# Performance work log

Hardware: AMD Instinct MI355X
Metric: run time of the kernel (lower is better)

## Reference

```python
import jax, jax.numpy as jnp
import numpy as np

D = 256          # B == num_experts == hidden_dim == input_dim (required by the module's broadcasting)
NUM_HEADS = 4
LN_EPS = 1e-5


def _layer_norm(x, g, b):
    mu = jnp.mean(x, axis=-1, keepdims=True)
    var = jnp.mean(jnp.square(x - mu), axis=-1, keepdims=True)
    return (x - mu) * jax.lax.rsqrt(var + LN_EPS) * g + b


def setup_inputs() -> dict:
    key = jax.random.key(0)
    ks = jax.random.split(key, 12)
    B = E = H = IN = D
    s = 0.02
    return {
        "x": jax.random.normal(ks[0], (B, IN), jnp.float32),
        "task_embedding": jax.random.normal(ks[1], (B, H), jnp.float32),
        # stacked per-expert params: Linear(IN,H) -> LayerNorm(H) -> ReLU -> Linear(H,H)
        "W1": jax.random.normal(ks[2], (E, H, IN), jnp.float32) * s,
        "b1": jnp.zeros((E, H), jnp.float32),
        "ln1_g": jnp.ones((E, H), jnp.float32),
        "ln1_b": jnp.zeros((E, H), jnp.float32),
        "W2": jax.random.normal(ks[3], (E, H, H), jnp.float32) * s,
        "b2": jnp.zeros((E, H), jnp.float32),
        # MultiheadAttention in-projection (packed q,k,v). v/out_proj are dead code
        # in this forward (attn_output is discarded) but v slice kept for faithful shapes.
        "in_proj_w": jax.random.normal(ks[4], (3 * H, H), jnp.float32) * s,
        "in_proj_b": jnp.zeros((3 * H,), jnp.float32),
        # combine: Linear(H,H) -> LayerNorm(H) -> ReLU
        "cw": jax.random.normal(ks[5], (H, H), jnp.float32) * s,
        "cb": jnp.zeros((H,), jnp.float32),
        "cg": jnp.ones((H,), jnp.float32),
        "cbeta": jnp.zeros((H,), jnp.float32),
    }


def reference(x, task_embedding, W1, b1, ln1_g, ln1_b, W2, b2,
              in_proj_w, in_proj_b, cw, cb, cg, cbeta):
    B, H = x.shape
    hd = H // NUM_HEADS

    # ---- all experts on the same input (batched over expert axis) ----
    h = jnp.einsum('bi,eoi->beo', x, W1) + b1          # [B,E,H]
    h = _layer_norm(h, ln1_g, ln1_b)
    h = jax.nn.relu(h)
    eo = jnp.einsum('beh,eoh->beo', h, W2) + b2        # [B,E,H] expert_outputs

    # ---- attention gate (only attn_weights are used downstream) ----
    Wq, Wk = in_proj_w[:H], in_proj_w[H:2 * H]
    bq, bk = in_proj_b[:H], in_proj_b[H:2 * H]
    q = (task_embedding @ Wq.T + bq).reshape(B, NUM_HEADS, hd) / jnp.sqrt(jnp.float32(hd))
    k = (jnp.einsum('beh,oh->beo', eo, Wk) + bk).reshape(B, -1, NUM_HEADS, hd)
    scores = jnp.einsum('bnd,bend->bne', q, k)          # [B, heads, E]
    attn = jax.nn.softmax(scores, axis=-1)
    weights = jnp.mean(attn, axis=1)                    # [B, E] (avg over heads)

    # ---- faithful torch broadcasting of [B,E,H] * [1,B,E] (requires B==E==H) ----
    # combined[b,h] = sum_e eo[b,e,h] * weights[e,h]
    combined = jnp.einsum('beh,eh->bh', eo, weights)

    out = jax.nn.relu(_layer_norm(combined @ cw.T + cb, cg, cbeta))
    return out, weights[:, None, :], eo
```

## Files before the change

kernel.cpp:

```cpp
#include <hip/hip_runtime.h>

typedef _Float16 f16_t;
typedef f16_t f16x8 __attribute__((ext_vector_type(8)));
typedef float f32x4 __attribute__((ext_vector_type(4)));

#define MFMA16(a,b,c) __builtin_amdgcn_mfma_f32_16x16x32_f16(a,b,c,0,0,0)
#define VM0 asm volatile("s_waitcnt vmcnt(0)" ::: "memory")
#define VM2 asm volatile("s_waitcnt vmcnt(2)" ::: "memory")

__device__ __forceinline__ void cp16(const void* g, void* l){
  __builtin_amdgcn_global_load_lds(
      (const __attribute__((address_space(1))) void*)g,
      (__attribute__((address_space(3))) void*)l, 16, 0, 0);
}

__device__ __forceinline__ f16x8 cvt8h(float4 a, float4 b){
  f16x8 r;
  r[0]=(f16_t)a.x; r[1]=(f16_t)a.y; r[2]=(f16_t)a.z; r[3]=(f16_t)a.w;
  r[4]=(f16_t)b.x; r[5]=(f16_t)b.y; r[6]=(f16_t)b.z; r[7]=(f16_t)b.w;
  return r;
}

template<int NT>
__device__ __forceinline__ void stage_f16(const float* __restrict__ src,
                                          char* dst, int rows, int tid){
  const int nchunk = rows * 32;
  const float4* s4 = reinterpret_cast<const float4*>(src);
  for (int cid = tid; cid < nchunk; cid += NT){
    int r = cid >> 5, c = cid & 31;
    *reinterpret_cast<f16x8*>(dst + r*512 + ((c ^ (r&7))<<4)) = cvt8h(s4[cid*2], s4[cid*2+1]);
  }
}

__device__ __forceinline__ f16x8 ldsA(const char* buf, int row, int c16){
  return *reinterpret_cast<const f16x8*>(buf + row*512 + ((c16 ^ (row&7))<<4));
}

__device__ __forceinline__ void issue_tile(const f16_t* wsrc, int kb, char* wt, int lane){
  const f16_t* s = wsrc + kb*32;
  char* d = wt + (kb&1)*2048 + lane*16;
  cp16(s, d);
  cp16(s + 16*256, d + 1024);
}

__device__ __forceinline__ void gemm_pipe(f32x4 acc[4][2], const char* bufA,
    const f16_t* wsrc, char* wt, int lane, int lo16, int hi4){
  #pragma unroll
  for (int kb = 0; kb < 8; ++kb){
    if (kb < 7) { VM2; } else { VM0; }
    const char* ws = wt + (kb&1)*2048 + lo16*64 + hi4*16;
    f16x8 bf0 = *reinterpret_cast<const f16x8*>(ws);
    f16x8 bf1 = *reinterpret_cast<const f16x8*>(ws + 1024);
    #pragma unroll
    for (int mb = 0; mb < 4; ++mb){
      f16x8 af = ldsA(bufA, mb*16 + lo16, kb*4 + hi4);
      acc[mb][0] = MFMA16(af, bf0, acc[mb][0]);
      acc[mb][1] = MFMA16(af, bf1, acc[mb][1]);
    }
    __builtin_amdgcn_sched_barrier(0);
    if (kb + 2 < 8) issue_tile(wsrc, kb + 2, wt, lane);
  }
}

__device__ __forceinline__ void gemm_w32(f32x4 acc[4][2], const char* bufA,
    const float* __restrict__ W, int n0, int lo16, int hi4){
  #pragma unroll
  for (int kb = 0; kb < 8; ++kb){
    f16x8 bf[2];
    #pragma unroll
    for (int nb = 0; nb < 2; ++nb){
      const float4* p = reinterpret_cast<const float4*>(W + ((n0 + nb*16 + lo16)<<8) + kb*32 + hi4*8);
      bf[nb] = cvt8h(p[0], p[1]);
    }
    #pragma unroll
    for (int mb = 0; mb < 4; ++mb){
      f16x8 af = ldsA(bufA, mb*16 + lo16, kb*4 + hi4);
      acc[mb][0] = MFMA16(af, bf[0], acc[mb][0]);
      acc[mb][1] = MFMA16(af, bf[1], acc[mb][1]);
    }
  }
}

__global__ __launch_bounds__(256)
void k0_cvt(const float* __restrict__ W1, const float* __restrict__ W2,
            const float* __restrict__ Wk, f16_t* __restrict__ w1h,
            f16_t* __restrict__ w2h, f16_t* __restrict__ wkh)
{
  const long long NG1 = 2097152, NG2 = 4194304, NGT = 4202496;
  for (long long gidx = (long long)blockIdx.x*256 + threadIdx.x; gidx < NGT;
       gidx += (long long)gridDim.x*256){
    const float4* s; f16_t* d; long long off;
    if (gidx < NG1){ s = (const float4*)W1; d = w1h; off = gidx; }
    else if (gidx < NG2){ s = (const float4*)W2; d = w2h; off = gidx - NG1; }
    else { s = (const float4*)Wk; d = wkh; off = gidx - NG2; }
    *reinterpret_cast<f16x8*>(d + off*8) = cvt8h(s[off*2], s[off*2+1]);
  }
}

template<int W16>
__global__ __launch_bounds__(512, 4)
void k2_fused(const float* __restrict__ x, const void* __restrict__ W1v,
              const float* __restrict__ b1, const float* __restrict__ g1,
              const float* __restrict__ bb1, const void* __restrict__ W2v,
              const float* __restrict__ b2, const void* __restrict__ Wkv,
              const float* __restrict__ ipb, const float* __restrict__ q,
              float* __restrict__ eo_out, float* __restrict__ scores)
{
  __shared__ __align__(16) char lds[70144];
  char* bufA = lds;
  float* red = (float*)(lds + 32768);
  float* st  = (float*)(lds + 36864);
  char* wpipe = lds + 37376;

  const int l = blockIdx.x;
  const int e    = (l & 7) * 32 + (l >> 5);
  const int b0   = ((l >> 3) & 3) * 64;
  const int tid = threadIdx.x;
  const int lane = tid & 63, wid = tid >> 6;
  const int lo16 = lane & 15, hi4 = lane >> 4;
  const int n0 = wid * 32;
  char* wt = wpipe + wid*4096;

  const int r_in = lane >> 2, c_in = (lane & 3) * 8;
  const f16_t* src1 = nullptr; const f16_t* src2 = nullptr; const f16_t* srcK = nullptr;
  if (W16){
    src1 = (const f16_t*)W1v + e*65536 + (n0 + r_in)*256 + c_in;
    src2 = (const f16_t*)W2v + e*65536 + (n0 + r_in)*256 + c_in;
    srcK = (const f16_t*)Wkv +           (n0 + r_in)*256 + c_in;
    issue_tile(src1, 0, wt, lane);
    issue_tile(src1, 1, wt, lane);
  }

  stage_f16<512>(x + b0*256, bufA, 64, tid);
  __syncthreads();

  f32x4 acc[4][2];
  #pragma unroll
  for (int mb=0;mb<4;++mb){
    #pragma unroll
    for (int nb=0;nb<2;++nb) acc[mb][nb] = (f32x4)0.0f;
  }

  if (W16) gemm_pipe(acc, bufA, src1, wt, lane, lo16, hi4);
  else     gemm_w32(acc, bufA, (const float*)W1v + e*65536, n0, lo16, hi4);

  if (W16){
    issue_tile(src2, 0, wt, lane);
    issue_tile(src2, 1, wt, lane);
  }

  float b1v[2], g1v[2], bbv[2];
  #pragma unroll
  for (int nb=0;nb<2;++nb){
    int c = n0 + nb*16 + lo16;
    b1v[nb] = b1[e*256 + c];
    g1v[nb] = g1[e*256 + c];
    bbv[nb] = bb1[e*256 + c];
  }
  #pragma unroll
  for (int mb=0;mb<4;++mb){
    #pragma unroll
    for (int nb=0;nb<2;++nb){
      #pragma unroll
      for (int r=0;r<4;++r) acc[mb][nb][r] += b1v[nb];
    }
  }

  #pragma unroll
  for (int mb=0;mb<4;++mb){
    #pragma unroll
    for (int r=0;r<4;++r){
      float s=0.f, ss=0.f;
      #pragma unroll
      for (int nb=0;nb<2;++nb){ float v = acc[mb][nb][r]; s += v; ss += v*v; }
      #pragma unroll
      for (int m=1;m<16;m<<=1){ s += __shfl_xor(s, m, 64); ss += __shfl_xor(ss, m, 64); }
      if (lo16 == 0){
        int row = mb*16 + hi4*4 + r;
        red[row*16 + wid]     = s;
        red[row*16 + 8 + wid] = ss;
      }
    }
  }
  __syncthreads();
  if (tid < 64){
    float s  = 0.f, ss = 0.f;
    #pragma unroll
    for (int i=0;i<8;++i){ s += red[tid*16 + i]; ss += red[tid*16 + 8 + i]; }
    float mu = s * (1.f/256.f);
    float var = ss * (1.f/256.f) - mu*mu;
    st[tid*2]   = mu;
    st[tid*2+1] = rsqrtf(var + 1e-5f);
  }
  __syncthreads();

  #pragma unroll
  for (int mb=0;mb<4;++mb){
    #pragma unroll
    for (int r=0;r<4;++r){
      int row = mb*16 + hi4*4 + r;
      float mu = st[row*2], rs = st[row*2+1];
      #pragma unroll
      for (int nb=0;nb<2;++nb){
        int c = n0 + nb*16 + lo16;
        float v = (acc[mb][nb][r] - mu) * rs * g1v[nb] + bbv[nb];
        v = fmaxf(v, 0.f);
        int off = row*512 + (((c>>3) ^ (row&7))<<4) + (c&7)*2;
        *reinterpret_cast<f16_t*>(bufA + off) = (f16_t)v;
      }
    }
  }
  __syncthreads();

  #pragma unroll
  for (int mb=0;mb<4;++mb){
    #pragma unroll
    for (int nb=0;nb<2;++nb) acc[mb][nb] = (f32x4)0.0f;
  }
  if (W16) gemm_pipe(acc, bufA, src2, wt, lane, lo16, hi4);
  else     gemm_w32(acc, bufA, (const float*)W2v + e*65536, n0, lo16, hi4);

  float b2v[2];
  #pragma unroll
  for (int nb=0;nb<2;++nb) b2v[nb] = b2[e*256 + n0 + nb*16 + lo16];

  __syncthreads();

  if (W16){
    issue_tile(srcK, 0, wt, lane);
    issue_tile(srcK, 1, wt, lane);
  }

  #pragma unroll
  for (int mb=0;mb<4;++mb){
    #pragma unroll
    for (int r=0;r<4;++r){
      int row = mb*16 + hi4*4 + r;
      int b = b0 + row;
      #pragma unroll
      for (int nb=0;nb<2;++nb){
        int c = n0 + nb*16 + lo16;
        float v = acc[mb][nb][r] + b2v[nb];
        eo_out[(b*256 + e)*256 + c] = v;
        int off = row*512 + (((c>>3) ^ (row&7))<<4) + (c&7)*2;
        *reinterpret_cast<f16_t*>(bufA + off) = (f16_t)v;
      }
    }
  }
  __syncthreads();

  #pragma unroll
  for (int mb=0;mb<4;++mb){
    #pragma unroll
    for (int nb=0;nb<2;++nb) acc[mb][nb] = (f32x4)0.0f;
  }
  if (W16) gemm_pipe(acc, bufA, srcK, wt, lane, lo16, hi4);
  else     gemm_w32(acc, bufA, (const float*)Wkv, n0, lo16, hi4);

  float bkv[2];
  #pragma unroll
  for (int nb=0;nb<2;++nb) bkv[nb] = ipb[256 + n0 + nb*16 + lo16];

  #pragma unroll
  for (int mb=0;mb<4;++mb){
    #pragma unroll
    for (int r=0;r<4;++r){
      int row = mb*16 + hi4*4 + r;
      int b = b0 + row;
      float p = 0.f;
      #pragma unroll
      for (int nb=0;nb<2;++nb){
        int c = n0 + nb*16 + lo16;
        p += q[b*256 + c] * (acc[mb][nb][r] + bkv[nb]);
      }
      #pragma unroll
      for (int m=1;m<16;m<<=1) p += __shfl_xor(p, m, 64);
      if (lo16 == 0) red[row*16 + wid] = p;
    }
  }
  __syncthreads();
  if (tid < 256){
    int row = tid >> 2, hd = tid & 3;
    float sc = red[row*16 + hd*2] + red[row*16 + hd*2 + 1];
    scores[((b0 + row)*4 + hd)*256 + e] = sc;
  }
}

__global__ __launch_bounds__(512, 4)
void k_mini(const float* __restrict__ A, const float* __restrict__ W,
            const float* __restrict__ bias, float scale, int do_ln,
            const float* __restrict__ g, const float* __restrict__ bb,
            int do_relu, float* __restrict__ out)
{
  __shared__ __align__(16) char lds[18688];
  char* bufA = lds;
  float* red = (float*)(lds + 16384);
  float* st  = (float*)(lds + 18432);

  const int b0 = blockIdx.x * 32;
  const int tid = threadIdx.x;
  const int lane = tid & 63, wid = tid >> 6;
  const int lo16 = lane & 15, hi4 = lane >> 4;
  const int n0 = wid * 32;

  stage_f16<512>(A + b0*256, bufA, 32, tid);
  __syncthreads();

  f32x4 acc[2][2];
  #pragma unroll
  for (int mb=0;mb<2;++mb){
    #pragma unroll
    for (int nb=0;nb<2;++nb) acc[mb][nb] = (f32x4)0.0f;
  }
  #pragma unroll
  for (int kb = 0; kb < 8; ++kb){
    f16x8 bf[2];
    #pragma unroll
    for (int nb = 0; nb < 2; ++nb){
      const float4* p = reinterpret_cast<const float4*>(W + ((n0 + nb*16 + lo16)<<8) + kb*32 + hi4*8);
      bf[nb] = cvt8h(p[0], p[1]);
    }
    #pragma unroll
    for (int mb = 0; mb < 2; ++mb){
      f16x8 af = ldsA(bufA, mb*16 + lo16, kb*4 + hi4);
      acc[mb][0] = MFMA16(af, bf[0], acc[mb][0]);
      acc[mb][1] = MFMA16(af, bf[1], acc[mb][1]);
    }
  }

  float bv[2], gv[2], bbv[2];
  #pragma unroll
  for (int nb=0;nb<2;++nb){
    int c = n0 + nb*16 + lo16;
    bv[nb]  = bias[c];
    gv[nb]  = do_ln ? g[c]  : 1.f;
    bbv[nb] = do_ln ? bb[c] : 0.f;
  }
  #pragma unroll
  for (int mb=0;mb<2;++mb){
    #pragma unroll
    for (int nb=0;nb<2;++nb){
      #pragma unroll
      for (int r=0;r<4;++r) acc[mb][nb][r] = (acc[mb][nb][r] + bv[nb]) * scale;
    }
  }

  if (do_ln){
    #pragma unroll
    for (int mb=0;mb<2;++mb){
      #pragma unroll
      for (int r=0;r<4;++r){
        float s=0.f, ss=0.f;
        #pragma unroll
        for (int nb=0;nb<2;++nb){ float v = acc[mb][nb][r]; s += v; ss += v*v; }
        #pragma unroll
        for (int m=1;m<16;m<<=1){ s += __shfl_xor(s, m, 64); ss += __shfl_xor(ss, m, 64); }
        if (lo16 == 0){
          int row = mb*16 + hi4*4 + r;
          red[row*16 + wid]     = s;
          red[row*16 + 8 + wid] = ss;
        }
      }
    }
    __syncthreads();
    if (tid < 32){
      float s = 0.f, ss = 0.f;
      #pragma unroll
      for (int i=0;i<8;++i){ s += red[tid*16 + i]; ss += red[tid*16 + 8 + i]; }
      float mu = s * (1.f/256.f);
      float var = ss * (1.f/256.f) - mu*mu;
      st[tid*2]   = mu;
      st[tid*2+1] = rsqrtf(var + 1e-5f);
    }
    __syncthreads();
  }

  #pragma unroll
  for (int mb=0;mb<2;++mb){
    #pragma unroll
    for (int r=0;r<4;++r){
      int row = mb*16 + hi4*4 + r;
      float mu = 0.f, rs = 1.f;
      if (do_ln){ mu = st[row*2]; rs = st[row*2+1]; }
      #pragma unroll
      for (int nb=0;nb<2;++nb){
        int c = n0 + nb*16 + lo16;
        float v = acc[mb][nb][r];
        if (do_ln) v = (v - mu) * rs * gv[nb] + bbv[nb];
        if (do_relu) v = fmaxf(v, 0.f);
        out[(b0 + row)*256 + c] = v;
      }
    }
  }
}

__global__ __launch_bounds__(256)
void k3_softmax(const float* __restrict__ scores, float* __restrict__ wts)
{
  const int b = blockIdx.x, t = threadIdx.x;
  const int wid = t >> 6, lane = t & 63;
  __shared__ float r4[4];
  float sc[4];
  #pragma unroll
  for (int n=0;n<4;++n) sc[n] = scores[(b*4 + n)*256 + t];
  float wsum = 0.f;
  for (int n=0;n<4;++n){
    float m = sc[n];
    #pragma unroll
    for (int k=1;k<64;k<<=1) m = fmaxf(m, __shfl_xor(m, k, 64));
    if (lane == 0) r4[wid] = m;
    __syncthreads();
    m = fmaxf(fmaxf(r4[0], r4[1]), fmaxf(r4[2], r4[3]));
    __syncthreads();
    float ex = __expf(sc[n] - m);
    float s = ex;
    #pragma unroll
    for (int k=1;k<64;k<<=1) s += __shfl_xor(s, k, 64);
    if (lane == 0) r4[wid] = s;
    __syncthreads();
    s = r4[0] + r4[1] + r4[2] + r4[3];
    __syncthreads();
    wsum += ex / s;
  }
  wts[b*256 + t] = wsum * 0.25f;
}

__global__ __launch_bounds__(1024)
void k4a_combined(const float* __restrict__ eo, const float* __restrict__ wts,
                  float* __restrict__ cmb)
{
  __shared__ float part[1024];
  const int b = blockIdx.x, t = threadIdx.x;
  const int c = t >> 8, h = t & 255;
  const float* p = eo + b*65536 + h;
  float s = 0.f;
  #pragma unroll 8
  for (int i = 0; i < 64; ++i){
    int e2 = c*64 + i;
    s += p[e2*256] * wts[e2*256 + h];
  }
  part[t] = s;
  __syncthreads();
  if (t < 256) cmb[b*256 + t] = part[t] + part[t+256] + part[t+512] + part[t+768];
}

extern "C" void kernel_launch(void* const* d_in, const int* in_sizes, int n_in,
                              void* d_out, int out_size, void* d_ws, size_t ws_size,
                              hipStream_t stream)
{
  const float* x    = (const float*)d_in[0];
  const float* te   = (const float*)d_in[1];
  const float* W1   = (const float*)d_in[2];
  const float* b1   = (const float*)d_in[3];
  const float* g1   = (const float*)d_in[4];
  const float* bb1  = (const float*)d_in[5];
  const float* W2   = (const float*)d_in[6];
  const float* b2   = (const float*)d_in[7];
  const float* ipw  = (const float*)d_in[8];
  const float* ipb  = (const float*)d_in[9];
  const float* cw   = (const float*)d_in[10];
  const float* cb   = (const float*)d_in[11];
  const float* cg   = (const float*)d_in[12];
  const float* cbt  = (const float*)d_in[13];

  float* out    = (float*)d_out;
  float* wts    = out + 65536;
  float* eo     = out + 131072;

  const size_t F16_BYTES = 2ull*(16777216ull*2 + 65536);
  const size_t NEED = F16_BYTES + 4ull*(65536 + 262144 + 65536);
  const bool f16w = ws_size >= NEED;

  f16_t* w1h = (f16_t*)d_ws;
  f16_t* w2h = w1h + 16777216;
  f16_t* wkh = w2h + 16777216;
  float* fbase = f16w ? (float*)((char*)d_ws + F16_BYTES) : (float*)d_ws;
  float* q      = fbase;
  float* scores = q + 65536;
  float* cmb    = scores + 262144;

  k_mini<<<8, 512, 0, stream>>>(te, ipw, ipb, 0.125f, 0, nullptr, nullptr, 0, q);

  if (f16w){
    k0_cvt<<<2048, 256, 0, stream>>>(W1, W2, ipw + 65536, w1h, w2h, wkh);
    k2_fused<1><<<1024, 512, 0, stream>>>(x, w1h, b1, g1, bb1, w2h, b2,
                                          wkh, ipb, q, eo, scores);
  } else {
    k2_fused<0><<<1024, 512, 0, stream>>>(x, W1, b1, g1, bb1, W2, b2,
                                          ipw + 65536, ipb, q, eo, scores);
  }

  k3_softmax<<<256, 256, 0, stream>>>(scores, wts);
  k4a_combined<<<256, 1024, 0, stream>>>(eo, wts, cmb);
  k_mini<<<8, 512, 0, stream>>>(cmb, cw, cb, 1.0f, 1, cg, cbt, 1, out);
}
```

Measured before the change: 143.6 us.

## Stream fp32 weights directly into LDS and drop separate f16 conversion kernel

Removes the pre-pass kernel that converted W1, W2 and Wk to fp16 in workspace. The fused kernel now copies fp32 weight tiles straight into LDS with async global-to-LDS loads and converts them to fp16 in registers just before the MFMAs. The pipeline is deepened to three stages, and the bias loads are hoisted to the start of the kernel. This saves the extra read and write pass over about 128MB of weights, but each GEMM now reads twice the bytes, and the larger LDS footprint cuts occupancy to 2 blocks per CU.

```diff
diff --git a/kernel.cpp b/kernel.cpp
--- a/kernel.cpp
+++ b/kernel.cpp
@@ -6,7 +6,8 @@
 
 #define MFMA16(a,b,c) __builtin_amdgcn_mfma_f32_16x16x32_f16(a,b,c,0,0,0)
 #define VM0 asm volatile("s_waitcnt vmcnt(0)" ::: "memory")
-#define VM2 asm volatile("s_waitcnt vmcnt(2)" ::: "memory")
+#define VM4 asm volatile("s_waitcnt vmcnt(4)" ::: "memory")
+#define VM8 asm volatile("s_waitcnt vmcnt(8)" ::: "memory")
 
 __device__ __forceinline__ void cp16(const void* g, void* l){
   __builtin_amdgcn_global_load_lds(
@@ -36,21 +37,27 @@
   return *reinterpret_cast<const f16x8*>(buf + row*512 + ((c16 ^ (row&7))<<4));
 }
 
-__device__ __forceinline__ void issue_tile(const f16_t* wsrc, int kb, char* wt, int lane){
-  const f16_t* s = wsrc + kb*32;
-  char* d = wt + (kb&1)*2048 + lane*16;
-  cp16(s, d);
-  cp16(s + 16*256, d + 1024);
+__device__ __forceinline__ void issue_tile(const float* wsrc_lane, int kb, char* wt, int lane){
+  const float* s = wsrc_lane + kb*32;
+  char* d = wt + (kb%3)*4096 + lane*16;
+  cp16(s,              d);
+  cp16(s + 4,          d + 1024);
+  cp16(s + 16*256,     d + 2048);
+  cp16(s + 16*256 + 4, d + 3072);
 }
 
 __device__ __forceinline__ void gemm_pipe(f32x4 acc[4][2], const char* bufA,
-    const f16_t* wsrc, char* wt, int lane, int lo16, int hi4){
+    const float* wsrc_lane, char* wt, int lane, int lo16, int hi4){
   #pragma unroll
   for (int kb = 0; kb < 8; ++kb){
-    if (kb < 7) { VM2; } else { VM0; }
-    const char* ws = wt + (kb&1)*2048 + lo16*64 + hi4*16;
-    f16x8 bf0 = *reinterpret_cast<const f16x8*>(ws);
-    f16x8 bf1 = *reinterpret_cast<const f16x8*>(ws + 1024);
+    if (kb < 6) { VM8; } else if (kb == 6) { VM4; } else { VM0; }
+    const char* ws = wt + (kb%3)*4096 + lane*16;
+    float4 w00 = *reinterpret_cast<const float4*>(ws);
+    float4 w01 = *reinterpret_cast<const float4*>(ws + 1024);
+    float4 w10 = *reinterpret_cast<const float4*>(ws + 2048);
+    float4 w11 = *reinterpret_cast<const float4*>(ws + 3072);
+    f16x8 bf0 = cvt8h(w00, w01);
+    f16x8 bf1 = cvt8h(w10, w11);
     #pragma unroll
     for (int mb = 0; mb < 4; ++mb){
       f16x8 af = ldsA(bufA, mb*16 + lo16, kb*4 + hi4);
@@ -58,55 +65,19 @@
       acc[mb][1] = MFMA16(af, bf1, acc[mb][1]);
     }
     __builtin_amdgcn_sched_barrier(0);
-    if (kb + 2 < 8) issue_tile(wsrc, kb + 2, wt, lane);
-  }
-}
-
-__device__ __forceinline__ void gemm_w32(f32x4 acc[4][2], const char* bufA,
-    const float* __restrict__ W, int n0, int lo16, int hi4){
-  #pragma unroll
-  for (int kb = 0; kb < 8; ++kb){
-    f16x8 bf[2];
-    #pragma unroll
-    for (int nb = 0; nb < 2; ++nb){
-      const float4* p = reinterpret_cast<const float4*>(W + ((n0 + nb*16 + lo16)<<8) + kb*32 + hi4*8);
-      bf[nb] = cvt8h(p[0], p[1]);
-    }
-    #pragma unroll
-    for (int mb = 0; mb < 4; ++mb){
-      f16x8 af = ldsA(bufA, mb*16 + lo16, kb*4 + hi4);
-      acc[mb][0] = MFMA16(af, bf[0], acc[mb][0]);
-      acc[mb][1] = MFMA16(af, bf[1], acc[mb][1]);
-    }
-  }
-}
-
-__global__ __launch_bounds__(256)
-void k0_cvt(const float* __restrict__ W1, const float* __restrict__ W2,
-            const float* __restrict__ Wk, f16_t* __restrict__ w1h,
-            f16_t* __restrict__ w2h, f16_t* __restrict__ wkh)
-{
-  const long long NG1 = 2097152, NG2 = 4194304, NGT = 4202496;
-  for (long long gidx = (long long)blockIdx.x*256 + threadIdx.x; gidx < NGT;
-       gidx += (long long)gridDim.x*256){
-    const float4* s; f16_t* d; long long off;
-    if (gidx < NG1){ s = (const float4*)W1; d = w1h; off = gidx; }
-    else if (gidx < NG2){ s = (const float4*)W2; d = w2h; off = gidx - NG1; }
-    else { s = (const float4*)Wk; d = wkh; off = gidx - NG2; }
-    *reinterpret_cast<f16x8*>(d + off*8) = cvt8h(s[off*2], s[off*2+1]);
-  }
-}
-
-template<int W16>
-__global__ __launch_bounds__(512, 4)
-void k2_fused(const float* __restrict__ x, const void* __restrict__ W1v,
+    if (kb + 3 < 8) issue_tile(wsrc_lane, kb + 3, wt, lane);
+  }
+}
+
+__global__ __launch_bounds__(512, 2)
+void k2_fused(const float* __restrict__ x, const float* __restrict__ W1,
               const float* __restrict__ b1, const float* __restrict__ g1,
-              const float* __restrict__ bb1, const void* __restrict__ W2v,
-              const float* __restrict__ b2, const void* __restrict__ Wkv,
+              const float* __restrict__ bb1, const float* __restrict__ W2,
+              const float* __restrict__ b2, const float* __restrict__ Wk,
               const float* __restrict__ ipb, const float* __restrict__ q,
               float* __restrict__ eo_out, float* __restrict__ scores)
 {
-  __shared__ __align__(16) char lds[70144];
+  __shared__ __align__(16) char lds[135680];
   char* bufA = lds;
   float* red = (float*)(lds + 32768);
   float* st  = (float*)(lds + 36864);
@@ -119,44 +90,44 @@
   const int lane = tid & 63, wid = tid >> 6;
   const int lo16 = lane & 15, hi4 = lane >> 4;
   const int n0 = wid * 32;
-  char* wt = wpipe + wid*4096;
-
-  const int r_in = lane >> 2, c_in = (lane & 3) * 8;
-  const f16_t* src1 = nullptr; const f16_t* src2 = nullptr; const f16_t* srcK = nullptr;
-  if (W16){
-    src1 = (const f16_t*)W1v + e*65536 + (n0 + r_in)*256 + c_in;
-    src2 = (const f16_t*)W2v + e*65536 + (n0 + r_in)*256 + c_in;
-    srcK = (const f16_t*)Wkv +           (n0 + r_in)*256 + c_in;
-    issue_tile(src1, 0, wt, lane);
-    issue_tile(src1, 1, wt, lane);
-  }
-
-  stage_f16<512>(x + b0*256, bufA, 64, tid);
-  __syncthreads();
-
-  f32x4 acc[4][2];
-  #pragma unroll
-  for (int mb=0;mb<4;++mb){
-    #pragma unroll
-    for (int nb=0;nb<2;++nb) acc[mb][nb] = (f32x4)0.0f;
-  }
-
-  if (W16) gemm_pipe(acc, bufA, src1, wt, lane, lo16, hi4);
-  else     gemm_w32(acc, bufA, (const float*)W1v + e*65536, n0, lo16, hi4);
-
-  if (W16){
-    issue_tile(src2, 0, wt, lane);
-    issue_tile(src2, 1, wt, lane);
-  }
-
-  float b1v[2], g1v[2], bbv[2];
+  char* wt = wpipe + wid*12288;
+
+  const int pl = (n0 + (lane & 15))*256 + (lane >> 4)*8;
+  const float* src1 = W1 + e*65536 + pl;
+  const float* src2 = W2 + e*65536 + pl;
+  const float* srcK = Wk + pl;
+
+  issue_tile(src1, 0, wt, lane);
+  issue_tile(src1, 1, wt, lane);
+  issue_tile(src1, 2, wt, lane);
+
+  float b1v[2], g1v[2], bbv[2], b2v[2], bkv[2];
   #pragma unroll
   for (int nb=0;nb<2;++nb){
     int c = n0 + nb*16 + lo16;
     b1v[nb] = b1[e*256 + c];
     g1v[nb] = g1[e*256 + c];
     bbv[nb] = bb1[e*256 + c];
-  }
+    b2v[nb] = b2[e*256 + c];
+    bkv[nb] = ipb[256 + c];
+  }
+
+  stage_f16<512>(x + b0*256, bufA, 64, tid);
+  __syncthreads();
+
+  f32x4 acc[4][2];
+  #pragma unroll
+  for (int mb=0;mb<4;++mb){
+    #pragma unroll
+    for (int nb=0;nb<2;++nb) acc[mb][nb] = (f32x4)0.0f;
+  }
+
+  gemm_pipe(acc, bufA, src1, wt, lane, lo16, hi4);
+
+  issue_tile(src2, 0, wt, lane);
+  issue_tile(src2, 1, wt, lane);
+  issue_tile(src2, 2, wt, lane);
+
   #pragma unroll
   for (int mb=0;mb<4;++mb){
     #pragma unroll
@@ -217,19 +188,13 @@
     #pragma unroll
     for (int nb=0;nb<2;++nb) acc[mb][nb] = (f32x4)0.0f;
   }
-  if (W16) gemm_pipe(acc, bufA, src2, wt, lane, lo16, hi4);
-  else     gemm_w32(acc, bufA, (const float*)W2v + e*65536, n0, lo16, hi4);
-
-  float b2v[2];
-  #pragma unroll
-  for (int nb=0;nb<2;++nb) b2v[nb] = b2[e*256 + n0 + nb*16 + lo16];
-
-  __syncthreads();
-
-  if (W16){
-    issue_tile(srcK, 0, wt, lane);
-    issue_tile(srcK, 1, wt, lane);
-  }
+  gemm_pipe(acc, bufA, src2, wt, lane, lo16, hi4);
+
+  __syncthreads();
+
+  issue_tile(srcK, 0, wt, lane);
+  issue_tile(srcK, 1, wt, lane);
+  issue_tile(srcK, 2, wt, lane);
 
   #pragma unroll
   for (int mb=0;mb<4;++mb){
@@ -254,12 +219,7 @@
     #pragma unroll
     for (int nb=0;nb<2;++nb) acc[mb][nb] = (f32x4)0.0f;
   }
-  if (W16) gemm_pipe(acc, bufA, srcK, wt, lane, lo16, hi4);
-  else     gemm_w32(acc, bufA, (const float*)Wkv, n0, lo16, hi4);
-
-  float bkv[2];
-  #pragma unroll
-  for (int nb=0;nb<2;++nb) bkv[nb] = ipb[256 + n0 + nb*16 + lo16];
+  gemm_pipe(acc, bufA, srcK, wt, lane, lo16, hi4);
 
   #pragma unroll
   for (int mb=0;mb<4;++mb){
@@ -467,29 +427,13 @@
   float* wts    = out + 65536;
   float* eo     = out + 131072;
 
-  const size_t F16_BYTES = 2ull*(16777216ull*2 + 65536);
-  const size_t NEED = F16_BYTES + 4ull*(65536 + 262144 + 65536);
-  const bool f16w = ws_size >= NEED;
-
-  f16_t* w1h = (f16_t*)d_ws;
-  f16_t* w2h = w1h + 16777216;
-  f16_t* wkh = w2h + 16777216;
-  float* fbase = f16w ? (float*)((char*)d_ws + F16_BYTES) : (float*)d_ws;
-  float* q      = fbase;
+  float* q      = (float*)d_ws;
   float* scores = q + 65536;
   float* cmb    = scores + 262144;
 
   k_mini<<<8, 512, 0, stream>>>(te, ipw, ipb, 0.125f, 0, nullptr, nullptr, 0, q);
-
-  if (f16w){
-    k0_cvt<<<2048, 256, 0, stream>>>(W1, W2, ipw + 65536, w1h, w2h, wkh);
-    k2_fused<1><<<1024, 512, 0, stream>>>(x, w1h, b1, g1, bb1, w2h, b2,
-                                          wkh, ipb, q, eo, scores);
-  } else {
-    k2_fused<0><<<1024, 512, 0, stream>>>(x, W1, b1, g1, bb1, W2, b2,
-                                          ipw + 65536, ipb, q, eo, scores);
-  }
-
+  k2_fused<<<1024, 512, 0, stream>>>(x, W1, b1, g1, bb1, W2, b2,
+                                     ipw + 65536, ipb, q, eo, scores);
   k3_softmax<<<256, 256, 0, stream>>>(scores, wts);
   k4a_combined<<<256, 1024, 0, stream>>>(eo, wts, cmb);
   k_mini<<<8, 512, 0, stream>>>(cmb, cw, cb, 1.0f, 1, cg, cbt, 1, out);
```

Result: slower. 188.4 us (+31.2%).
